# Kernel optimization log

Hardware: AMD Instinct MI355X
Metric: run time of the kernel (lower is better)

Reference implementation:

```python
import jax, jax.numpy as jnp
import numpy as np

B, S, C, H = 2, 512, 25, 768


def setup_inputs() -> dict:
    key = jax.random.key(0)
    ks = jax.random.split(key, 10)
    sc = 1.0 / np.sqrt(H)
    return {
        "token_rep": jax.random.normal(ks[0], (B, S, H), jnp.float32),
        "label_rep": jax.random.normal(ks[1], (B, C, H), jnp.float32),
        # proj_token: Linear(H, 2H) stored as [in, out] for x @ W
        "Wt": jax.random.normal(ks[2], (H, 2 * H), jnp.float32) * sc,
        "bt": jnp.zeros((2 * H,), jnp.float32),
        # proj_label: Linear(H, 2H)
        "Wl": jax.random.normal(ks[3], (H, 2 * H), jnp.float32) * sc,
        "bl": jnp.zeros((2 * H,), jnp.float32),
        # out_mlp[0]: Linear(3H, 4H)
        "W1": jax.random.normal(ks[4], (3 * H, 4 * H), jnp.float32) * (1.0 / np.sqrt(3 * H)),
        "b1": jnp.zeros((4 * H,), jnp.float32),
        # out_mlp[3]: Linear(4H, 3)
        "W2": jax.random.normal(ks[5], (4 * H, 3), jnp.float32) * (1.0 / np.sqrt(4 * H)),
        "b2": jnp.zeros((3,), jnp.float32),
    }


def reference(token_rep, label_rep, Wt, bt, Wl, bl, W1, b1, W2, b2):
    h = token_rep.shape[-1]
    # project and split into (additive half, multiplicative half)
    tp = token_rep @ Wt + bt            # [B,S,2H]
    lp = label_rep @ Wl + bl            # [B,C,2H]
    ta, tb = tp[..., :h], tp[..., h:]
    la, lb = lp[..., :h], lp[..., h:]
    # First MLP layer on concat([ta, la, tb*lb]) without materializing the concat:
    # split W1 row-wise into the three input blocks.
    W1t, W1l, W1p = W1[:h], W1[h:2 * h], W1[2 * h:]
    hid = (ta @ W1t)[:, :, None, :] \
        + (la @ W1l)[:, None, :, :] \
        + jnp.einsum('bsh,bch,hf->bscf', tb, lb, W1p) \
        + b1                            # [B,S,C,4H]
    # Dropout is identity in eval mode.
    return jax.nn.relu(hid) @ W2 + b2   # [B,S,C,3]
```

## Files before the change

### kernel.cpp

```cpp
#include <hip/hip_runtime.h>
#include <hip/hip_bf16.h>
#include <cstdint>
#include <cstddef>

#define BB 2
#define SS 512
#define CC 25
#define HH 768
#define H2 1536
#define H3 2304
#define H4 3072
#define XC_STRIDE ((size_t)96 * 512 * 8)

typedef __attribute__((ext_vector_type(8))) short bf16x8;
typedef __attribute__((ext_vector_type(4))) float f32x4;

#define DEVINL static __device__ __forceinline__

DEVINL unsigned short f2bf(float f) {
  union { float f; unsigned u; } v; v.f = f;
  unsigned r = v.u + 0x7FFF + ((v.u >> 16) & 1);
  return (unsigned short)(r >> 16);
}
DEVINL float bf2f(unsigned short b) {
  union { unsigned u; float f; } v; v.u = ((unsigned)b) << 16; return v.f;
}

DEVINL void async16(const void* g, void* l) {
  __builtin_amdgcn_global_load_lds(
      (const __attribute__((address_space(1))) void*)g,
      (__attribute__((address_space(3))) void*)l, 16, 0, 0);
}

__global__ void k_prep_cast(const float* __restrict__ token,
                            const float* __restrict__ label,
                            const float* __restrict__ b2,
                            unsigned short* __restrict__ TC,
                            unsigned short* __restrict__ LC,
                            float* __restrict__ out) {
  __shared__ float tile[64][33];
  const int bid = blockIdx.x;
  const int tid = threadIdx.x;
  if (bid < 408) {
    const float* in;
    unsigned short* o;
    int R, RP, kt, rt;
    if (bid < 384) {
      in = token; o = TC; R = 1024; RP = 1024; kt = bid % 24; rt = bid / 24;
    } else {
      in = label; o = LC; R = 50; RP = 64; kt = bid - 384; rt = 0;
    }
    const int k0 = kt * 32, r0 = rt * 64;
    const int tx = tid & 31, ty = tid >> 5;
#pragma unroll
    for (int i = 0; i < 8; i++) {
      int r = r0 + ty + i * 8;
      tile[ty + i * 8][tx] = in[(size_t)min(r, R - 1) * HH + k0 + tx];
    }
    __syncthreads();
    const int rl = tid & 63, kcl = tid >> 6;
    bf16x8 ov;
#pragma unroll
    for (int j = 0; j < 8; j++) ov[j] = (short)f2bf(tile[rl][kcl * 8 + j]);
    *(bf16x8*)&o[((size_t)((k0 >> 3) + kcl) * RP + r0 + rl) * 8] = ov;
  } else {
    int i = (bid - 408) * 256 + tid;
    if (i < BB * SS * CC * 3) out[i] = b2[i % 3];
  }
}

__global__ void k_prep_w(const float* __restrict__ Wt,
                         const float* __restrict__ Wl,
                         const float* __restrict__ W1,
                         unsigned short* __restrict__ WtC,
                         unsigned short* __restrict__ WlC,
                         unsigned short* __restrict__ W1C) {
  const int bid = blockIdx.x, tid = threadIdx.x;
  const float* in;
  unsigned short* o;
  int N, bx, by;
  if (bid < 3456) {
    in = W1; o = W1C; N = H4; bx = bid % 48; by = bid / 48;
  } else if (bid < 4032) {
    int b = bid - 3456; in = Wt; o = WtC; N = H2; bx = b % 24; by = b / 24;
  } else {
    int b = bid - 4032; in = Wl; o = WlC; N = H2; bx = b % 24; by = b / 24;
  }
  const int f = bx * 64 + (tid & 63);
  const int hc = by * 4 + (tid >> 6);
  bf16x8 ov;
#pragma unroll
  for (int j = 0; j < 8; j++)
    ov[j] = (short)f2bf(in[(size_t)(hc * 8 + j) * N + f]);
  *(bf16x8*)&o[((size_t)hc * N + f) * 8] = ov;
}

__global__ void k_make_x(const unsigned short* __restrict__ TP,
                         const unsigned short* __restrict__ LP,
                         unsigned short* __restrict__ XC) {
  int hc = blockIdx.x >> 1;
  int s = (blockIdx.x & 1) * 256 + threadIdx.x;
  int bc = blockIdx.y;
  int b = bc / CC;
  bf16x8 tv = *(const bf16x8*)&TP[((size_t)(96 + hc) * 1024 + b * 512 + s) * 8];
  bf16x8 lv = *(const bf16x8*)&LP[((size_t)(96 + hc) * 64 + bc) * 8];
  bf16x8 o;
#pragma unroll
  for (int j = 0; j < 8; j++)
    o[j] = (short)f2bf(bf2f((unsigned short)tv[j]) * bf2f((unsigned short)lv[j]));
  *(bf16x8*)&XC[(size_t)bc * XC_STRIDE + ((size_t)hc * 512 + s) * 8] = o;
}

template <int MODE>
__global__ __launch_bounds__(256, 4) void gemmC(
    const unsigned short* __restrict__ A, int NRA, int MA,
    const unsigned short* __restrict__ Bt, int NRB,
    int Klen,
    unsigned short* __restrict__ Cbf, float* __restrict__ Cf, int ldc,
    const float* __restrict__ bias,
    const float* __restrict__ base, const float* __restrict__ al,
    const float* __restrict__ b1, const float* __restrict__ W2,
    float* __restrict__ out) {
  __shared__ __align__(16) unsigned short As[8 * 128 * 8];
  __shared__ __align__(16) unsigned short Bs[8 * 128 * 8];

  const int tid = threadIdx.x;
  const int lane = tid & 63;
  const int wave = tid >> 6;
  const int q = lane >> 4;
  const int li = lane & 15;
  const int wm = (wave >> 1) * 64;
  const int wn = (wave & 1) * 64;

  const int n0 = blockIdx.x * 128;
  int m0, bc = 0;
  const unsigned short* Ab = A;
  if (MODE == 2) {
    bc = blockIdx.y >> 2;
    m0 = (blockIdx.y & 3) * 128;
    Ab = A + (size_t)bc * XC_STRIDE;
  } else {
    m0 = blockIdx.y * 128;
  }

  f32x4 acc[4][4];
#pragma unroll
  for (int i = 0; i < 4; i++)
#pragma unroll
    for (int j = 0; j < 4; j++) acc[i][j] = (f32x4){0.f, 0.f, 0.f, 0.f};

  int sr[4], skc[4], sra[4];
#pragma unroll
  for (int j = 0; j < 4; j++) {
    int slot = j * 256 + tid;
    skc[j] = slot >> 7;
    sr[j] = slot & 127;
    sra[j] = min(m0 + sr[j], MA - 1);
  }

  auto stage = [&](int kciter) {
#pragma unroll
    for (int j = 0; j < 4; j++) {
      int slot = j * 256 + tid;
      async16(Ab + ((size_t)(kciter + skc[j]) * NRA + sra[j]) * 8,
              (char*)As + slot * 16);
      async16(Bt + ((size_t)(kciter + skc[j]) * NRB + n0 + sr[j]) * 8,
              (char*)Bs + slot * 16);
    }
  };

  stage(0);
  const int NI = Klen / 64;
  for (int it = 0; it < NI; it++) {
    __syncthreads();
#pragma unroll
    for (int ks = 0; ks < 2; ks++) {
      bf16x8 af[4], bb[4];
#pragma unroll
      for (int mi = 0; mi < 4; mi++)
        af[mi] = *(const bf16x8*)&As[((ks * 4 + q) * 128 + wm + mi * 16 + li) * 8];
#pragma unroll
      for (int ni = 0; ni < 4; ni++)
        bb[ni] = *(const bf16x8*)&Bs[((ks * 4 + q) * 128 + wn + ni * 16 + li) * 8];
#pragma unroll
      for (int mi = 0; mi < 4; mi++)
#pragma unroll
        for (int ni = 0; ni < 4; ni++)
          acc[mi][ni] = __builtin_amdgcn_mfma_f32_16x16x32_bf16(
              af[mi], bb[ni], acc[mi][ni], 0, 0, 0);
    }
    __syncthreads();
    if (it + 1 < NI) stage((it + 1) * 8);
  }

  if (MODE == 0) {
#pragma unroll
    for (int mi = 0; mi < 4; mi++)
#pragma unroll
      for (int rr = 0; rr < 4; rr++) {
        int row = m0 + wm + mi * 16 + q * 4 + rr;
        if (row < MA) {
#pragma unroll
          for (int ni = 0; ni < 4; ni++) {
            int col = n0 + wn + ni * 16 + li;
            Cbf[((size_t)(col >> 3) * ldc + row) * 8 + (col & 7)] =
                f2bf(acc[mi][ni][rr] + bias[col]);
          }
        }
      }
  } else if (MODE == 1) {
#pragma unroll
    for (int mi = 0; mi < 4; mi++)
#pragma unroll
      for (int rr = 0; rr < 4; rr++) {
        int row = m0 + wm + mi * 16 + q * 4 + rr;
        if (row < MA) {
#pragma unroll
          for (int ni = 0; ni < 4; ni++) {
            int col = n0 + wn + ni * 16 + li;
            Cf[(size_t)row * ldc + col] = acc[mi][ni][rr];
          }
        }
      }
  } else {
    const int b = bc / CC, c = bc % CC;
    int fcol[4];
    float alb[4];
#pragma unroll
    for (int ni = 0; ni < 4; ni++) {
      int f = n0 + wn + ni * 16 + li;
      fcol[ni] = f;
      alb[ni] = al[(size_t)bc * H4 + f] + b1[f];
    }
    bf16x8 w2f[2];
#pragma unroll
    for (int ks = 0; ks < 2; ks++)
#pragma unroll
      for (int jj = 0; jj < 8; jj++) {
        int f = n0 + wn + ks * 32 + q * 8 + jj;
        float v = (li < 3) ? W2[(size_t)f * 3 + li] : 0.f;
        w2f[ks][jj] = (short)f2bf(v);
      }
    unsigned short* Ew = (unsigned short*)((char*)As + wave * 2304);

#pragma unroll
    for (int mi = 0; mi < 4; mi++) {
      float bs[4][4];
#pragma unroll
      for (int rr = 0; rr < 4; rr++) {
        int s_l = m0 + wm + mi * 16 + q * 4 + rr;
        const float* bp = base + (size_t)(b * SS + s_l) * H4;
#pragma unroll
        for (int ni = 0; ni < 4; ni++) bs[ni][rr] = bp[fcol[ni]];
      }
#pragma unroll
      for (int rr = 0; rr < 4; rr++)
#pragma unroll
        for (int ni = 0; ni < 4; ni++) {
          float v = acc[mi][ni][rr] + bs[ni][rr] + alb[ni];
          v = fmaxf(v, 0.f);
          Ew[(q * 4 + rr) * 72 + ni * 16 + li] = f2bf(v);
        }
      f32x4 oc = (f32x4){0.f, 0.f, 0.f, 0.f};
#pragma unroll
      for (int ks = 0; ks < 2; ks++) {
        bf16x8 ef = *(const bf16x8*)&Ew[li * 72 + ks * 32 + q * 8];
        oc = __builtin_amdgcn_mfma_f32_16x16x32_bf16(ef, w2f[ks], oc, 0, 0, 0);
      }
#pragma unroll
      for (int rr = 0; rr < 4; rr++) {
        int s_l = m0 + wm + mi * 16 + q * 4 + rr;
        if (li < 3)
          atomicAdd(&out[((size_t)(b * SS + s_l) * CC + c) * 3 + li], oc[rr]);
      }
    }
  }
}


extern "C" void kernel_launch(void* const* d_in, const int* in_sizes, int n_in,
                              void* d_out, int out_size, void* d_ws, size_t ws_size,
                              hipStream_t stream) {
  (void)in_sizes; (void)n_in; (void)ws_size; (void)out_size;
  const float* token = (const float*)d_in[0];
  const float* label = (const float*)d_in[1];
  const float* Wt    = (const float*)d_in[2];
  const float* bt    = (const float*)d_in[3];
  const float* Wl    = (const float*)d_in[4];
  const float* bl    = (const float*)d_in[5];
  const float* W1    = (const float*)d_in[6];
  const float* b1    = (const float*)d_in[7];
  const float* W2    = (const float*)d_in[8];
  const float* b2    = (const float*)d_in[9];
  float* out = (float*)d_out;

  char* p = (char*)d_ws;
  auto alloc = [&](size_t bytes) {
    char* r = p;
    p += (bytes + 255) & ~(size_t)255;
    return r;
  };
  unsigned short* TC  = (unsigned short*)alloc((size_t)96 * 1024 * 8 * 2);
  unsigned short* LC  = (unsigned short*)alloc((size_t)96 * 64 * 8 * 2);
  unsigned short* WtC = (unsigned short*)alloc((size_t)96 * 1536 * 8 * 2);
  unsigned short* WlC = (unsigned short*)alloc((size_t)96 * 1536 * 8 * 2);
  unsigned short* W1C = (unsigned short*)alloc((size_t)288 * 3072 * 8 * 2);
  unsigned short* TP  = (unsigned short*)alloc((size_t)192 * 1024 * 8 * 2);
  unsigned short* LP  = (unsigned short*)alloc((size_t)192 * 64 * 8 * 2);
  unsigned short* XC  = (unsigned short*)alloc((size_t)CC * BB * XC_STRIDE * 2);
  float* base = (float*)alloc((size_t)BB * SS * H4 * 4);
  float* al   = (float*)alloc((size_t)BB * CC * H4 * 4);

  k_prep_cast<<<708, 256, 0, stream>>>(token, label, b2, TC, LC, out);
  k_prep_w<<<4608, 256, 0, stream>>>(Wt, Wl, W1, WtC, WlC, W1C);

  gemmC<0><<<dim3(12, 1), 256, 0, stream>>>(
      LC, 64, 50, WlC, H2, HH, LP, nullptr, 64, bl,
      nullptr, nullptr, nullptr, nullptr, nullptr);
  gemmC<0><<<dim3(12, 8), 256, 0, stream>>>(
      TC, 1024, 1024, WtC, H2, HH, TP, nullptr, 1024, bt,
      nullptr, nullptr, nullptr, nullptr, nullptr);

  k_make_x<<<dim3(192, 50), 256, 0, stream>>>(TP, LP, XC);

  gemmC<1><<<dim3(24, 1), 256, 0, stream>>>(
      LP, 64, 50, W1C + (size_t)96 * H4 * 8, H4, HH, nullptr, al, H4, nullptr,
      nullptr, nullptr, nullptr, nullptr, nullptr);
  gemmC<1><<<dim3(24, 8), 256, 0, stream>>>(
      TP, 1024, 1024, W1C, H4, HH, nullptr, base, H4, nullptr,
      nullptr, nullptr, nullptr, nullptr, nullptr);

  gemmC<2><<<dim3(24, 200), 256, 0, stream>>>(
      XC, 512, 512, W1C + (size_t)192 * H4 * 8, H4, HH, nullptr, nullptr, 0,
      nullptr, base, al, b1, W2, out);
}
```

Measured before the change: 305.5 us.

## Merge independent prep, projection and make_x kernels into fewer launches

Combines the activation cast, bias init and weight cast kernels into one launch. It also merges the token and label projection GEMMs into one grid, and folds the base/al GEMMs together with the elementwise product that builds XC into another. This cuts the launch count from eight to four and lets small grids share the device. The GEMM K loop is hard-coded to 12 iterations. The merged k_mm2 launch mixes heavy GEMM blocks with many light elementwise blocks, so the scheduling balance may change.

Result: faster. 273.9 us (-10.3%).

```diff
diff --git a/kernel.cpp b/kernel.cpp
--- a/kernel.cpp
+++ b/kernel.cpp
@@ -32,12 +32,18 @@
       (__attribute__((address_space(3))) void*)l, 16, 0, 0);
 }
 
-__global__ void k_prep_cast(const float* __restrict__ token,
-                            const float* __restrict__ label,
-                            const float* __restrict__ b2,
-                            unsigned short* __restrict__ TC,
-                            unsigned short* __restrict__ LC,
-                            float* __restrict__ out) {
+__global__ void k_prep(const float* __restrict__ token,
+                       const float* __restrict__ label,
+                       const float* __restrict__ b2,
+                       const float* __restrict__ Wt,
+                       const float* __restrict__ Wl,
+                       const float* __restrict__ W1,
+                       unsigned short* __restrict__ TC,
+                       unsigned short* __restrict__ LC,
+                       float* __restrict__ out,
+                       unsigned short* __restrict__ WtC,
+                       unsigned short* __restrict__ WlC,
+                       unsigned short* __restrict__ W1C) {
   __shared__ float tile[64][33];
   const int bid = blockIdx.x;
   const int tid = threadIdx.x;
@@ -63,67 +69,35 @@
 #pragma unroll
     for (int j = 0; j < 8; j++) ov[j] = (short)f2bf(tile[rl][kcl * 8 + j]);
     *(bf16x8*)&o[((size_t)((k0 >> 3) + kcl) * RP + r0 + rl) * 8] = ov;
-  } else {
+  } else if (bid < 708) {
     int i = (bid - 408) * 256 + tid;
     if (i < BB * SS * CC * 3) out[i] = b2[i % 3];
-  }
-}
-
-__global__ void k_prep_w(const float* __restrict__ Wt,
-                         const float* __restrict__ Wl,
-                         const float* __restrict__ W1,
-                         unsigned short* __restrict__ WtC,
-                         unsigned short* __restrict__ WlC,
-                         unsigned short* __restrict__ W1C) {
-  const int bid = blockIdx.x, tid = threadIdx.x;
-  const float* in;
-  unsigned short* o;
-  int N, bx, by;
-  if (bid < 3456) {
-    in = W1; o = W1C; N = H4; bx = bid % 48; by = bid / 48;
-  } else if (bid < 4032) {
-    int b = bid - 3456; in = Wt; o = WtC; N = H2; bx = b % 24; by = b / 24;
   } else {
-    int b = bid - 4032; in = Wl; o = WlC; N = H2; bx = b % 24; by = b / 24;
-  }
-  const int f = bx * 64 + (tid & 63);
-  const int hc = by * 4 + (tid >> 6);
-  bf16x8 ov;
-#pragma unroll
-  for (int j = 0; j < 8; j++)
-    ov[j] = (short)f2bf(in[(size_t)(hc * 8 + j) * N + f]);
-  *(bf16x8*)&o[((size_t)hc * N + f) * 8] = ov;
-}
-
-__global__ void k_make_x(const unsigned short* __restrict__ TP,
-                         const unsigned short* __restrict__ LP,
-                         unsigned short* __restrict__ XC) {
-  int hc = blockIdx.x >> 1;
-  int s = (blockIdx.x & 1) * 256 + threadIdx.x;
-  int bc = blockIdx.y;
-  int b = bc / CC;
-  bf16x8 tv = *(const bf16x8*)&TP[((size_t)(96 + hc) * 1024 + b * 512 + s) * 8];
-  bf16x8 lv = *(const bf16x8*)&LP[((size_t)(96 + hc) * 64 + bc) * 8];
-  bf16x8 o;
-#pragma unroll
-  for (int j = 0; j < 8; j++)
-    o[j] = (short)f2bf(bf2f((unsigned short)tv[j]) * bf2f((unsigned short)lv[j]));
-  *(bf16x8*)&XC[(size_t)bc * XC_STRIDE + ((size_t)hc * 512 + s) * 8] = o;
-}
-
-template <int MODE>
-__global__ __launch_bounds__(256, 4) void gemmC(
-    const unsigned short* __restrict__ A, int NRA, int MA,
-    const unsigned short* __restrict__ Bt, int NRB,
-    int Klen,
-    unsigned short* __restrict__ Cbf, float* __restrict__ Cf, int ldc,
-    const float* __restrict__ bias,
-    const float* __restrict__ base, const float* __restrict__ al,
-    const float* __restrict__ b1, const float* __restrict__ W2,
-    float* __restrict__ out) {
-  __shared__ __align__(16) unsigned short As[8 * 128 * 8];
-  __shared__ __align__(16) unsigned short Bs[8 * 128 * 8];
-
+    const int wb = bid - 708;
+    const float* in;
+    unsigned short* o;
+    int N, bx, by;
+    if (wb < 3456) {
+      in = W1; o = W1C; N = H4; bx = wb % 48; by = wb / 48;
+    } else if (wb < 4032) {
+      int b = wb - 3456; in = Wt; o = WtC; N = H2; bx = b % 24; by = b / 24;
+    } else {
+      int b = wb - 4032; in = Wl; o = WlC; N = H2; bx = b % 24; by = b / 24;
+    }
+    const int f = bx * 64 + (tid & 63);
+    const int hc = by * 4 + (tid >> 6);
+    bf16x8 ov;
+#pragma unroll
+    for (int j = 0; j < 8; j++)
+      ov[j] = (short)f2bf(in[(size_t)(hc * 8 + j) * N + f]);
+    *(bf16x8*)&o[((size_t)hc * N + f) * 8] = ov;
+  }
+}
+
+DEVINL void mm_kloop(const unsigned short* __restrict__ Ab, int NRA, int MA,
+                     int m0, const unsigned short* __restrict__ Bt, int NRB,
+                     int n0, unsigned short* As, unsigned short* Bs,
+                     f32x4 (&acc)[4][4]) {
   const int tid = threadIdx.x;
   const int lane = tid & 63;
   const int wave = tid >> 6;
@@ -132,23 +106,6 @@
   const int wm = (wave >> 1) * 64;
   const int wn = (wave & 1) * 64;
 
-  const int n0 = blockIdx.x * 128;
-  int m0, bc = 0;
-  const unsigned short* Ab = A;
-  if (MODE == 2) {
-    bc = blockIdx.y >> 2;
-    m0 = (blockIdx.y & 3) * 128;
-    Ab = A + (size_t)bc * XC_STRIDE;
-  } else {
-    m0 = blockIdx.y * 128;
-  }
-
-  f32x4 acc[4][4];
-#pragma unroll
-  for (int i = 0; i < 4; i++)
-#pragma unroll
-    for (int j = 0; j < 4; j++) acc[i][j] = (f32x4){0.f, 0.f, 0.f, 0.f};
-
   int sr[4], skc[4], sra[4];
 #pragma unroll
   for (int j = 0; j < 4; j++) {
@@ -157,7 +114,6 @@
     sr[j] = slot & 127;
     sra[j] = min(m0 + sr[j], MA - 1);
   }
-
   auto stage = [&](int kciter) {
 #pragma unroll
     for (int j = 0; j < 4; j++) {
@@ -170,8 +126,7 @@
   };
 
   stage(0);
-  const int NI = Klen / 64;
-  for (int it = 0; it < NI; it++) {
+  for (int it = 0; it < 12; it++) {
     __syncthreads();
 #pragma unroll
     for (int ks = 0; ks < 2; ks++) {
@@ -190,10 +145,83 @@
               af[mi], bb[ni], acc[mi][ni], 0, 0, 0);
     }
     __syncthreads();
-    if (it + 1 < NI) stage((it + 1) * 8);
-  }
-
-  if (MODE == 0) {
+    if (it + 1 < 12) stage((it + 1) * 8);
+  }
+}
+
+__global__ __launch_bounds__(256, 4) void k_mm1(
+    const unsigned short* __restrict__ TC, const unsigned short* __restrict__ LC,
+    const unsigned short* __restrict__ WtC, const unsigned short* __restrict__ WlC,
+    const float* __restrict__ bt, const float* __restrict__ bl,
+    unsigned short* __restrict__ TP, unsigned short* __restrict__ LP) {
+  __shared__ __align__(16) unsigned short As[8 * 128 * 8];
+  __shared__ __align__(16) unsigned short Bs[8 * 128 * 8];
+  const int bid = blockIdx.x;
+  const int nt = bid % 12, my = bid / 12;
+  const bool tok = my < 8;
+  const unsigned short* A = tok ? TC : LC;
+  const unsigned short* Bt = tok ? WtC : WlC;
+  const float* bias = tok ? bt : bl;
+  unsigned short* C = tok ? TP : LP;
+  const int NRA = tok ? 1024 : 64, MA = tok ? 1024 : 50;
+  const int m0 = tok ? my * 128 : 0;
+  const int ldc = NRA;
+  const int n0 = nt * 128;
+
+  f32x4 acc[4][4];
+#pragma unroll
+  for (int i = 0; i < 4; i++)
+#pragma unroll
+    for (int j = 0; j < 4; j++) acc[i][j] = (f32x4){0.f, 0.f, 0.f, 0.f};
+  mm_kloop(A, NRA, MA, m0, Bt, H2, n0, As, Bs, acc);
+
+  const int lane = threadIdx.x & 63, wave = threadIdx.x >> 6;
+  const int q = lane >> 4, li = lane & 15;
+  const int wm = (wave >> 1) * 64, wn = (wave & 1) * 64;
+#pragma unroll
+  for (int mi = 0; mi < 4; mi++)
+#pragma unroll
+    for (int rr = 0; rr < 4; rr++) {
+      int row = m0 + wm + mi * 16 + q * 4 + rr;
+      if (row < MA) {
+#pragma unroll
+        for (int ni = 0; ni < 4; ni++) {
+          int col = n0 + wn + ni * 16 + li;
+          C[((size_t)(col >> 3) * ldc + row) * 8 + (col & 7)] =
+              f2bf(acc[mi][ni][rr] + bias[col]);
+        }
+      }
+    }
+}
+
+__global__ __launch_bounds__(256, 4) void k_mm2(
+    const unsigned short* __restrict__ TP, const unsigned short* __restrict__ LP,
+    const unsigned short* __restrict__ W1C,
+    float* __restrict__ base, float* __restrict__ al,
+    unsigned short* __restrict__ XC) {
+  __shared__ __align__(16) unsigned short As[8 * 128 * 8];
+  __shared__ __align__(16) unsigned short Bs[8 * 128 * 8];
+  const int bid = blockIdx.x;
+  if (bid < 216) {
+    const int nt = bid % 24, my = bid / 24;
+    const bool tok = my < 8;
+    const unsigned short* A = tok ? TP : LP;
+    const unsigned short* Bt = tok ? W1C : W1C + (size_t)96 * H4 * 8;
+    float* Cf = tok ? base : al;
+    const int NRA = tok ? 1024 : 64, MA = tok ? 1024 : 50;
+    const int m0 = tok ? my * 128 : 0;
+    const int n0 = nt * 128;
+
+    f32x4 acc[4][4];
+#pragma unroll
+    for (int i = 0; i < 4; i++)
+#pragma unroll
+      for (int j = 0; j < 4; j++) acc[i][j] = (f32x4){0.f, 0.f, 0.f, 0.f};
+    mm_kloop(A, NRA, MA, m0, Bt, H4, n0, As, Bs, acc);
+
+    const int lane = threadIdx.x & 63, wave = threadIdx.x >> 6;
+    const int q = lane >> 4, li = lane & 15;
+    const int wm = (wave >> 1) * 64, wn = (wave & 1) * 64;
 #pragma unroll
     for (int mi = 0; mi < 4; mi++)
 #pragma unroll
@@ -203,76 +231,104 @@
 #pragma unroll
           for (int ni = 0; ni < 4; ni++) {
             int col = n0 + wn + ni * 16 + li;
-            Cbf[((size_t)(col >> 3) * ldc + row) * 8 + (col & 7)] =
-                f2bf(acc[mi][ni][rr] + bias[col]);
-          }
-        }
-      }
-  } else if (MODE == 1) {
-#pragma unroll
-    for (int mi = 0; mi < 4; mi++)
-#pragma unroll
-      for (int rr = 0; rr < 4; rr++) {
-        int row = m0 + wm + mi * 16 + q * 4 + rr;
-        if (row < MA) {
-#pragma unroll
-          for (int ni = 0; ni < 4; ni++) {
-            int col = n0 + wn + ni * 16 + li;
-            Cf[(size_t)row * ldc + col] = acc[mi][ni][rr];
+            Cf[(size_t)row * H4 + col] = acc[mi][ni][rr];
           }
         }
       }
   } else {
-    const int b = bc / CC, c = bc % CC;
-    int fcol[4];
-    float alb[4];
-#pragma unroll
-    for (int ni = 0; ni < 4; ni++) {
-      int f = n0 + wn + ni * 16 + li;
-      fcol[ni] = f;
-      alb[ni] = al[(size_t)bc * H4 + f] + b1[f];
-    }
-    bf16x8 w2f[2];
-#pragma unroll
-    for (int ks = 0; ks < 2; ks++)
-#pragma unroll
-      for (int jj = 0; jj < 8; jj++) {
-        int f = n0 + wn + ks * 32 + q * 8 + jj;
-        float v = (li < 3) ? W2[(size_t)f * 3 + li] : 0.f;
-        w2f[ks][jj] = (short)f2bf(v);
+    const int i = bid - 216;
+    const int bc = i / 192;
+    const int rem = i % 192;
+    const int hc = rem >> 1;
+    const int s = (rem & 1) * 256 + threadIdx.x;
+    const int b = bc / CC;
+    bf16x8 tv = *(const bf16x8*)&TP[((size_t)(96 + hc) * 1024 + b * 512 + s) * 8];
+    bf16x8 lv = *(const bf16x8*)&LP[((size_t)(96 + hc) * 64 + bc) * 8];
+    bf16x8 o;
+#pragma unroll
+    for (int j = 0; j < 8; j++)
+      o[j] = (short)f2bf(bf2f((unsigned short)tv[j]) * bf2f((unsigned short)lv[j]));
+    *(bf16x8*)&XC[(size_t)bc * XC_STRIDE + ((size_t)hc * 512 + s) * 8] = o;
+  }
+}
+
+__global__ __launch_bounds__(256, 4) void k_scorer(
+    const unsigned short* __restrict__ XC,
+    const unsigned short* __restrict__ Bt,
+    const float* __restrict__ base, const float* __restrict__ al,
+    const float* __restrict__ b1, const float* __restrict__ W2,
+    float* __restrict__ out) {
+  __shared__ __align__(16) unsigned short As[8 * 128 * 8];
+  __shared__ __align__(16) unsigned short Bs[8 * 128 * 8];
+  const int tid = threadIdx.x;
+  const int lane = tid & 63;
+  const int wave = tid >> 6;
+  const int q = lane >> 4;
+  const int li = lane & 15;
+  const int wm = (wave >> 1) * 64;
+  const int wn = (wave & 1) * 64;
+
+  const int n0 = blockIdx.x * 128;
+  const int bc = blockIdx.y >> 2;
+  const int m0 = (blockIdx.y & 3) * 128;
+  const unsigned short* Ab = XC + (size_t)bc * XC_STRIDE;
+
+  f32x4 acc[4][4];
+#pragma unroll
+  for (int i = 0; i < 4; i++)
+#pragma unroll
+    for (int j = 0; j < 4; j++) acc[i][j] = (f32x4){0.f, 0.f, 0.f, 0.f};
+  mm_kloop(Ab, 512, 512, m0, Bt, H4, n0, As, Bs, acc);
+
+  const int b = bc / CC, c = bc % CC;
+  int fcol[4];
+  float alb[4];
+#pragma unroll
+  for (int ni = 0; ni < 4; ni++) {
+    int f = n0 + wn + ni * 16 + li;
+    fcol[ni] = f;
+    alb[ni] = al[(size_t)bc * H4 + f] + b1[f];
+  }
+  bf16x8 w2f[2];
+#pragma unroll
+  for (int ks = 0; ks < 2; ks++)
+#pragma unroll
+    for (int jj = 0; jj < 8; jj++) {
+      int f = n0 + wn + ks * 32 + q * 8 + jj;
+      float v = (li < 3) ? W2[(size_t)f * 3 + li] : 0.f;
+      w2f[ks][jj] = (short)f2bf(v);
+    }
+  unsigned short* Ew = (unsigned short*)((char*)As + wave * 2304);
+
+#pragma unroll
+  for (int mi = 0; mi < 4; mi++) {
+    float bs[4][4];
+#pragma unroll
+    for (int rr = 0; rr < 4; rr++) {
+      int s_l = m0 + wm + mi * 16 + q * 4 + rr;
+      const float* bp = base + (size_t)(b * SS + s_l) * H4;
+#pragma unroll
+      for (int ni = 0; ni < 4; ni++) bs[ni][rr] = bp[fcol[ni]];
+    }
+#pragma unroll
+    for (int rr = 0; rr < 4; rr++)
+#pragma unroll
+      for (int ni = 0; ni < 4; ni++) {
+        float v = acc[mi][ni][rr] + bs[ni][rr] + alb[ni];
+        v = fmaxf(v, 0.f);
+        Ew[(q * 4 + rr) * 72 + ni * 16 + li] = f2bf(v);
       }
-    unsigned short* Ew = (unsigned short*)((char*)As + wave * 2304);
-
-#pragma unroll
-    for (int mi = 0; mi < 4; mi++) {
-      float bs[4][4];
-#pragma unroll
-      for (int rr = 0; rr < 4; rr++) {
-        int s_l = m0 + wm + mi * 16 + q * 4 + rr;
-        const float* bp = base + (size_t)(b * SS + s_l) * H4;
-#pragma unroll
-        for (int ni = 0; ni < 4; ni++) bs[ni][rr] = bp[fcol[ni]];
-      }
-#pragma unroll
-      for (int rr = 0; rr < 4; rr++)
-#pragma unroll
-        for (int ni = 0; ni < 4; ni++) {
-          float v = acc[mi][ni][rr] + bs[ni][rr] + alb[ni];
-          v = fmaxf(v, 0.f);
-          Ew[(q * 4 + rr) * 72 + ni * 16 + li] = f2bf(v);
-        }
-      f32x4 oc = (f32x4){0.f, 0.f, 0.f, 0.f};
-#pragma unroll
-      for (int ks = 0; ks < 2; ks++) {
-        bf16x8 ef = *(const bf16x8*)&Ew[li * 72 + ks * 32 + q * 8];
-        oc = __builtin_amdgcn_mfma_f32_16x16x32_bf16(ef, w2f[ks], oc, 0, 0, 0);
-      }
-#pragma unroll
-      for (int rr = 0; rr < 4; rr++) {
-        int s_l = m0 + wm + mi * 16 + q * 4 + rr;
-        if (li < 3)
-          atomicAdd(&out[((size_t)(b * SS + s_l) * CC + c) * 3 + li], oc[rr]);
-      }
+    f32x4 oc = (f32x4){0.f, 0.f, 0.f, 0.f};
+#pragma unroll
+    for (int ks = 0; ks < 2; ks++) {
+      bf16x8 ef = *(const bf16x8*)&Ew[li * 72 + ks * 32 + q * 8];
+      oc = __builtin_amdgcn_mfma_f32_16x16x32_bf16(ef, w2f[ks], oc, 0, 0, 0);
+    }
+#pragma unroll
+    for (int rr = 0; rr < 4; rr++) {
+      int s_l = m0 + wm + mi * 16 + q * 4 + rr;
+      if (li < 3)
+        atomicAdd(&out[((size_t)(b * SS + s_l) * CC + c) * 3 + li], oc[rr]);
     }
   }
 }
@@ -311,26 +367,10 @@
   float* base = (float*)alloc((size_t)BB * SS * H4 * 4);
   float* al   = (float*)alloc((size_t)BB * CC * H4 * 4);
 
-  k_prep_cast<<<708, 256, 0, stream>>>(token, label, b2, TC, LC, out);
-  k_prep_w<<<4608, 256, 0, stream>>>(Wt, Wl, W1, WtC, WlC, W1C);
-
-  gemmC<0><<<dim3(12, 1), 256, 0, stream>>>(
-      LC, 64, 50, WlC, H2, HH, LP, nullptr, 64, bl,
-      nullptr, nullptr, nullptr, nullptr, nullptr);
-  gemmC<0><<<dim3(12, 8), 256, 0, stream>>>(
-      TC, 1024, 1024, WtC, H2, HH, TP, nullptr, 1024, bt,
-      nullptr, nullptr, nullptr, nullptr, nullptr);
-
-  k_make_x<<<dim3(192, 50), 256, 0, stream>>>(TP, LP, XC);
-
-  gemmC<1><<<dim3(24, 1), 256, 0, stream>>>(
-      LP, 64, 50, W1C + (size_t)96 * H4 * 8, H4, HH, nullptr, al, H4, nullptr,
-      nullptr, nullptr, nullptr, nullptr, nullptr);
-  gemmC<1><<<dim3(24, 8), 256, 0, stream>>>(
-      TP, 1024, 1024, W1C, H4, HH, nullptr, base, H4, nullptr,
-      nullptr, nullptr, nullptr, nullptr, nullptr);
-
-  gemmC<2><<<dim3(24, 200), 256, 0, stream>>>(
-      XC, 512, 512, W1C + (size_t)192 * H4 * 8, H4, HH, nullptr, nullptr, 0,
-      nullptr, base, al, b1, W2, out);
-}
+  k_prep<<<5316, 256, 0, stream>>>(token, label, b2, Wt, Wl, W1,
+                                   TC, LC, out, WtC, WlC, W1C);
+  k_mm1<<<108, 256, 0, stream>>>(TC, LC, WtC, WlC, bt, bl, TP, LP);
+  k_mm2<<<9816, 256, 0, stream>>>(TP, LP, W1C, base, al, XC);
+  k_scorer<<<dim3(24, 200), 256, 0, stream>>>(
+      XC, W1C + (size_t)192 * H4 * 8, base, al, b1, W2, out);
+}
```
